# Kernel tuning notes

Measured on AMD Instinct MI355X. Metric: run time of the kernel, lower is better.

## Reference

```python
import jax, jax.numpy as jnp
import numpy as np

N = 50000      # nodes
E = 800000     # edges
IN = 128       # in_feats
HID = 16       # h_feats (per head)
HEADS = 8      # num_heads layer 1
CLS = 40       # num_classes
NEG_SLOPE = 0.2


def setup_inputs() -> dict:
    key = jax.random.key(0)
    ks = jax.random.split(key, 12)
    s = lambda fan: np.float32(1.0 / np.sqrt(fan))
    return {
        "features": jax.random.normal(ks[0], (N, IN), jnp.float32),
        "edge_src": jax.random.randint(ks[1], (E,), 0, N, dtype=jnp.int32),
        "edge_dst": jax.random.randint(ks[2], (E,), 0, N, dtype=jnp.int32),
        # layer 1 params
        "W1": jax.random.normal(ks[3], (IN, HEADS * HID), jnp.float32) * s(IN),
        "al1": jax.random.normal(ks[4], (HEADS, HID), jnp.float32) * s(HID),
        "ar1": jax.random.normal(ks[5], (HEADS, HID), jnp.float32) * s(HID),
        "b1": jnp.zeros((HEADS * HID,), jnp.float32),
        # layer 2 params (1 head)
        "W2": jax.random.normal(ks[6], (HEADS * HID, CLS), jnp.float32) * s(HEADS * HID),
        "al2": jax.random.normal(ks[7], (1, CLS), jnp.float32) * s(CLS),
        "ar2": jax.random.normal(ks[8], (1, CLS), jnp.float32) * s(CLS),
        "b2": jnp.zeros((CLS,), jnp.float32),
    }


def gat_conv(x, W, al, ar, b, src, dst, heads, out_dim):
    # x: [N, F_in] -> feat: [N, H, D]
    feat = (x @ W).reshape(-1, heads, out_dim)
    el = (feat * al).sum(-1)                      # [N, H]
    er = (feat * ar).sum(-1)                      # [N, H]
    e = jax.nn.leaky_relu(el[src] + er[dst], NEG_SLOPE)  # [E, H]
    # segment softmax over destination neighborhoods
    emax = jax.ops.segment_max(e, dst, num_segments=N)   # [N, H]
    emax = jnp.where(jnp.isfinite(emax), emax, jnp.float32(0.0))
    ee = jnp.exp(e - emax[dst])                   # [E, H]
    denom = jax.ops.segment_sum(ee, dst, num_segments=N)
    alpha = ee / (denom[dst] + jnp.float32(1e-9)) # [E, H]
    msg = alpha[:, :, None] * feat[src]           # [E, H, D]
    out = jax.ops.segment_sum(msg, dst, num_segments=N)  # [N, H, D]
    return out + b.reshape(1, heads, out_dim)


def reference(features, edge_src, edge_dst, W1, al1, ar1, b1, W2, al2, ar2, b2):
    h = jax.nn.elu(gat_conv(features, W1, al1, ar1, b1, edge_src, edge_dst, HEADS, HID))
    h = h.reshape(N, HEADS * HID)                 # flatten(1)
    out = gat_conv(h, W2, al2, ar2, b2, edge_src, edge_dst, 1, CLS)
    return out.mean(axis=1)                       # [N, CLS]
```

## Files before the change

### kernel.cpp

```cpp
#include <hip/hip_runtime.h>
#include <hip/hip_bf16.h>

#define N_NODES 50000
#define N_EDGES 800000
#define IN_F    128
#define HID     16
#define HEADS   8
#define F1      128
#define CLS     40
#define CLSP    64
#define NEG     0.2f
#define NEG_INF (-__builtin_inff())
#define SWEEPS      8
#define SWEEP_RANGE 6250
#define STRIDE      96

typedef __bf16 bf16x8 __attribute__((ext_vector_type(8)));
typedef float  f32x4  __attribute__((ext_vector_type(4)));
typedef float  f32x2  __attribute__((ext_vector_type(2)));

__device__ __forceinline__ float leaky(float v) { return v >= 0.0f ? v : NEG * v; }
__device__ __forceinline__ f32x2 unpk(unsigned u) {
    f32x2 r;
    r.x = __uint_as_float(u << 16);
    r.y = __uint_as_float(u & 0xffff0000u);
    return r;
}

__global__ void setup_kernel(const float* __restrict__ W1, const float* __restrict__ W2,
                             __bf16* __restrict__ w1t, __bf16* __restrict__ w2t,
                             int* __restrict__ cursor) {
    int i = blockIdx.x * blockDim.x + threadIdx.x;
    if (i < N_NODES) cursor[i] = 0;
    if (i < 128 * 128) {
        int n = i >> 7, k = i & 127;
        w1t[i] = (__bf16)W1[k * 128 + n];
    }
    if (i < CLSP * 128) {
        int n = i >> 7, k = i & 127;
        w2t[i] = (n < CLS) ? (__bf16)W2[k * CLS + n] : (__bf16)0.0f;
    }
}

__global__ void scatter_kernel(const int* __restrict__ src, const int* __restrict__ dst,
                               int* __restrict__ cursor, int* __restrict__ srcs_sorted) {
    const int BPS = (N_EDGES + 255) / 256;
    int sweep = blockIdx.x / BPS;
    int e = (blockIdx.x - sweep * BPS) * 256 + threadIdx.x;
    if (e >= N_EDGES) return;
    int d = dst[e];
    int lo = sweep * SWEEP_RANGE;
    if (d < lo || d >= lo + SWEEP_RANGE) return;
    int pos = d * STRIDE + atomicAdd(&cursor[d], 1);
    srcs_sorted[pos] = src[e];
}

__global__ __launch_bounds__(256) void gemm1_mfma(const float* __restrict__ A,
                                                  const __bf16* __restrict__ Wt,
                                                  const float* __restrict__ al1,
                                                  const float* __restrict__ ar1,
                                                  __bf16* __restrict__ outb,
                                                  float* __restrict__ el,
                                                  float* __restrict__ er) {
    int wave = threadIdx.x >> 6, lane = threadIdx.x & 63;
    int m0 = blockIdx.x * 64 + wave * 16;
    int c = lane & 15;
    int row = m0 + c;
    int rowc = row < N_NODES ? row : N_NODES - 1;
    int ko = (lane >> 4) * 8;

    f32x4 acc[8];
    #pragma unroll
    for (int t = 0; t < 8; ++t)
        #pragma unroll
        for (int r = 0; r < 4; ++r) acc[t][r] = 0.f;

    for (int ks = 0; ks < 128; ks += 32) {
        const float* ap = A + (size_t)rowc * 128 + ks + ko;
        float4 u = *(const float4*)ap;
        float4 v = *(const float4*)(ap + 4);
        bf16x8 a;
        a[0] = (__bf16)u.x; a[1] = (__bf16)u.y; a[2] = (__bf16)u.z; a[3] = (__bf16)u.w;
        a[4] = (__bf16)v.x; a[5] = (__bf16)v.y; a[6] = (__bf16)v.z; a[7] = (__bf16)v.w;
        #pragma unroll
        for (int t = 0; t < 8; ++t) {
            bf16x8 b = *(const bf16x8*)(Wt + (size_t)(t * 16 + c) * 128 + ks + ko);
            acc[t] = __builtin_amdgcn_mfma_f32_16x16x32_bf16(a, b, acc[t], 0, 0, 0);
        }
    }
    int rbase = m0 + (lane >> 4) * 4;
    #pragma unroll
    for (int t = 0; t < 8; ++t) {
        int gcol = t * 16 + c;
        #pragma unroll
        for (int r = 0; r < 4; ++r) {
            int grow = rbase + r;
            if (grow < N_NODES) outb[(size_t)grow * 128 + gcol] = (__bf16)acc[t][r];
        }
    }
    #pragma unroll
    for (int t = 0; t < 8; ++t) {
        float alv = al1[t * 16 + c];
        float arv = ar1[t * 16 + c];
        float pe[4], pr[4];
        #pragma unroll
        for (int r = 0; r < 4; ++r) { pe[r] = acc[t][r] * alv; pr[r] = acc[t][r] * arv; }
        #pragma unroll
        for (int mask = 1; mask <= 8; mask <<= 1) {
            #pragma unroll
            for (int r = 0; r < 4; ++r) {
                pe[r] += __shfl_xor(pe[r], mask, 64);
                pr[r] += __shfl_xor(pr[r], mask, 64);
            }
        }
        if (c == 0) {
            #pragma unroll
            for (int r = 0; r < 4; ++r) {
                int grow = rbase + r;
                if (grow < N_NODES) {
                    el[grow * 8 + t] = pe[r];
                    er[grow * 8 + t] = pr[r];
                }
            }
        }
    }
}

__global__ __launch_bounds__(256) void gemm2_mfma(const __bf16* __restrict__ A,
                                                  const __bf16* __restrict__ Wt,
                                                  const float* __restrict__ al2,
                                                  const float* __restrict__ ar2,
                                                  __bf16* __restrict__ out,
                                                  float* __restrict__ el,
                                                  float* __restrict__ er) {
    int wave = threadIdx.x >> 6, lane = threadIdx.x & 63;
    int m0 = blockIdx.x * 64 + wave * 16;
    int c = lane & 15;
    int row = m0 + c;
    int rowc = row < N_NODES ? row : N_NODES - 1;
    int ko = (lane >> 4) * 8;

    f32x4 acc[4];
    #pragma unroll
    for (int t = 0; t < 4; ++t)
        #pragma unroll
        for (int r = 0; r < 4; ++r) acc[t][r] = 0.f;

    for (int ks = 0; ks < 128; ks += 32) {
        bf16x8 a = *(const bf16x8*)(A + (size_t)rowc * 128 + ks + ko);
        #pragma unroll
        for (int t = 0; t < 4; ++t) {
            bf16x8 b = *(const bf16x8*)(Wt + (size_t)(t * 16 + c) * 128 + ks + ko);
            acc[t] = __builtin_amdgcn_mfma_f32_16x16x32_bf16(a, b, acc[t], 0, 0, 0);
        }
    }
    int rbase = m0 + (lane >> 4) * 4;
    #pragma unroll
    for (int t = 0; t < 4; ++t) {
        int gcol = t * 16 + c;
        #pragma unroll
        for (int r = 0; r < 4; ++r) {
            int grow = rbase + r;
            if (grow < N_NODES) out[(size_t)grow * CLSP + gcol] = (__bf16)acc[t][r];
        }
    }
    float pe[4] = {0.f, 0.f, 0.f, 0.f}, pr[4] = {0.f, 0.f, 0.f, 0.f};
    #pragma unroll
    for (int t = 0; t < 3; ++t) {
        int idx = t * 16 + c;
        float alv = (idx < CLS) ? al2[idx] : 0.f;
        float arv = (idx < CLS) ? ar2[idx] : 0.f;
        #pragma unroll
        for (int r = 0; r < 4; ++r) { pe[r] += acc[t][r] * alv; pr[r] += acc[t][r] * arv; }
    }
    #pragma unroll
    for (int mask = 1; mask <= 8; mask <<= 1) {
        #pragma unroll
        for (int r = 0; r < 4; ++r) {
            pe[r] += __shfl_xor(pe[r], mask, 64);
            pr[r] += __shfl_xor(pr[r], mask, 64);
        }
    }
    if (c == 0) {
        #pragma unroll
        for (int r = 0; r < 4; ++r) {
            int grow = rbase + r;
            if (grow < N_NODES) { el[grow] = pe[r]; er[grow] = pr[r]; }
        }
    }
}

__global__ __launch_bounds__(256) void gat1_fused(const int* __restrict__ degs,
                                                  const int* __restrict__ srcs,
                                                  const float* __restrict__ el,
                                                  const float* __restrict__ er,
                                                  const __bf16* __restrict__ feat1b,
                                                  const float* __restrict__ b1,
                                                  __bf16* __restrict__ hbufb) {
    __shared__ float a_lds[4][64 * 8];
    __shared__ int   s_lds[4][64];
    int wave = threadIdx.x >> 6;
    int lane = threadIdx.x & 63;
    int d = blockIdx.x * 4 + wave;
    int off = d * STRIDE;
    int deg = degs[d];

    int h = lane & 7, slot = lane >> 3;
    int q = lane >> 4, fg = lane & 15, hd = fg >> 1;
    float er_d = er[d * 8 + h];

    f32x2 accv[4];
    #pragma unroll
    for (int j = 0; j < 4; ++j) { accv[j].x = 0.f; accv[j].y = 0.f; }

    bool fast = (deg <= 64);
    if (fast) {
        int nit = (deg + 7) >> 3;
        float sc[8];
        int sreg[8];
        float m = NEG_INF;
        #pragma unroll
        for (int it = 0; it < 8; ++it) {
            float v = NEG_INF;
            int e = it * 8 + slot;
            if (it < nit && e < deg) {
                sreg[it] = srcs[off + e];
                v = leaky(el[sreg[it] * 8 + h] + er_d);
            }
            sc[it] = v;
            m = fmaxf(m, v);
        }
        float l = 0.f;
        #pragma unroll
        for (int it = 0; it < 8; ++it)
            l += (sc[it] == NEG_INF) ? 0.f : __expf(sc[it] - m);
        #pragma unroll
        for (int mask = 8; mask <= 32; mask <<= 1) {
            float m2 = __shfl_xor(m, mask, 64);
            float l2 = __shfl_xor(l, mask, 64);
            float mn = fmaxf(m, m2);
            float f1 = (m  == NEG_INF) ? 0.f : __expf(m - mn);
            float f2 = (m2 == NEG_INF) ? 0.f : __expf(m2 - mn);
            l = l * f1 + l2 * f2;
            m = mn;
        }
        float inv_l = 1.f / (l + 1e-9f);
        #pragma unroll
        for (int it = 0; it < 8; ++it) {
            int e = it * 8 + slot;
            if (it < nit && e < deg) {
                a_lds[wave][e * 8 + h] = __expf(sc[it] - m) * inv_l;
                if (h == 0) s_lds[wave][e] = sreg[it];
            }
        }
    }
    __syncthreads();

    if (fast) {
        int ng = (deg + 3) >> 2;
        #pragma unroll 4
        for (int g = 0; g < ng; ++g) {
            int k = g * 4 + q;
            float a = 0.f;
            int se = 0;
            if (k < deg) {
                a = a_lds[wave][k * 8 + hd];
                se = s_lds[wave][k];
            }
            uint4 p = *(const uint4*)(feat1b + (size_t)se * F1 + fg * 8);
            f32x2 av; av.x = a; av.y = a;
            accv[0] += av * unpk(p.x);
            accv[1] += av * unpk(p.y);
            accv[2] += av * unpk(p.z);
            accv[3] += av * unpk(p.w);
        }
    } else {
        float m = NEG_INF, l = 0.f;
        for (int base = 0; base < deg; base += 8) {
            int e = base + slot;
            float v = NEG_INF;
            if (e < deg) {
                int s = srcs[off + e];
                v = leaky(el[s * 8 + h] + er_d);
            }
            float mn = fmaxf(m, v);
            float f1 = (m == NEG_INF) ? 0.f : __expf(m - mn);
            float f2 = (v == NEG_INF) ? 0.f : __expf(v - mn);
            l = l * f1 + f2;
            m = mn;
        }
        #pragma unroll
        for (int mask = 8; mask <= 32; mask <<= 1) {
            float m2 = __shfl_xor(m, mask, 64);
            float l2 = __shfl_xor(l, mask, 64);
            float mn = fmaxf(m, m2);
            float f1 = (m  == NEG_INF) ? 0.f : __expf(m - mn);
            float f2 = (m2 == NEG_INF) ? 0.f : __expf(m2 - mn);
            l = l * f1 + l2 * f2;
            m = mn;
        }
        float inv_l = 1.f / (l + 1e-9f);

        for (int base = 0; base < deg; base += 8) {
            int e = base + slot;
            float alpha = 0.f;
            int s = 0;
            if (e < deg) {
                s = srcs[off + e];
                float v = leaky(el[s * 8 + h] + er_d);
                alpha = __expf(v - m) * inv_l;
            }
            #pragma unroll
            for (int sub = 0; sub < 2; ++sub) {
                int k = sub * 4 + q;
                float a  = __shfl(alpha, k * 8 + hd, 64);
                int   se = __shfl(s,     k * 8,      64);
                uint4 p = *(const uint4*)(feat1b + (size_t)se * F1 + fg * 8);
                f32x2 av; av.x = a; av.y = a;
                accv[0] += av * unpk(p.x);
                accv[1] += av * unpk(p.y);
                accv[2] += av * unpk(p.z);
                accv[3] += av * unpk(p.w);
            }
        }
    }

    float acc[8];
    #pragma unroll
    for (int j = 0; j < 4; ++j) { acc[2 * j] = accv[j].x; acc[2 * j + 1] = accv[j].y; }
    #pragma unroll
    for (int i = 0; i < 8; ++i) {
        acc[i] += __shfl_xor(acc[i], 16, 64);
        acc[i] += __shfl_xor(acc[i], 32, 64);
    }
    if (q == 0) {
        bf16x8 o;
        #pragma unroll
        for (int i = 0; i < 8; ++i) {
            float v = acc[i] + b1[fg * 8 + i];
            v = v > 0.f ? v : expm1f(v);
            o[i] = (__bf16)v;
        }
        *(bf16x8*)(hbufb + (size_t)d * F1 + fg * 8) = o;
    }
}

__global__ __launch_bounds__(256) void gat2_fused(const int* __restrict__ degs,
                                                  const int* __restrict__ srcs,
                                                  const float* __restrict__ el,
                                                  const float* __restrict__ er,
                                                  const __bf16* __restrict__ feat2p,
                                                  const float* __restrict__ b2,
                                                  float* __restrict__ out) {
    __shared__ float a_lds[4][64];
    __shared__ int   s_lds[4][64];
    int wave = threadIdx.x >> 6;
    int lane = threadIdx.x & 63;
    int d = blockIdx.x * 4 + wave;
    int off = d * STRIDE;
    int deg = degs[d];

    float er_d = er[d];
    bool fast = (deg <= 64);
    if (fast) {
        float sc = NEG_INF;
        int s0 = 0;
        if (lane < deg) {
            s0 = srcs[off + lane];
            sc = leaky(el[s0] + er_d);
        }
        float m = sc, l = (sc == NEG_INF) ? 0.f : 1.f;
        #pragma unroll
        for (int mask = 1; mask <= 32; mask <<= 1) {
            float m2 = __shfl_xor(m, mask, 64);
            float l2 = __shfl_xor(l, mask, 64);
            float mn = fmaxf(m, m2);
            float f1 = (m  == NEG_INF) ? 0.f : __expf(m - mn);
            float f2 = (m2 == NEG_INF) ? 0.f : __expf(m2 - mn);
            l = l * f1 + l2 * f2;
            m = mn;
        }
        float inv_l = 1.f / (l + 1e-9f);
        if (lane < deg) {
            a_lds[wave][lane] = __expf(sc - m) * inv_l;
            s_lds[wave][lane] = s0;
        }
    }
    __syncthreads();

    if (fast) {
        int q2  = lane >> 3;
        int cg8 = lane & 7;
        f32x2 accv[4];
        #pragma unroll
        for (int j = 0; j < 4; ++j) { accv[j].x = 0.f; accv[j].y = 0.f; }

        int ng = (deg + 7) >> 3;
        #pragma unroll 4
        for (int g = 0; g < ng; ++g) {
            int k = g * 8 + q2;
            float a = 0.f;
            int se = 0;
            if (k < deg) {
                a = a_lds[wave][k];
                se = s_lds[wave][k];
            }
            uint4 p = *(const uint4*)(feat2p + (size_t)se * CLSP + cg8 * 8);
            f32x2 av; av.x = a; av.y = a;
            accv[0] += av * unpk(p.x);
            accv[1] += av * unpk(p.y);
            accv[2] += av * unpk(p.z);
            accv[3] += av * unpk(p.w);
        }
        float acc[8];
        #pragma unroll
        for (int j = 0; j < 4; ++j) { acc[2 * j] = accv[j].x; acc[2 * j + 1] = accv[j].y; }
        #pragma unroll
        for (int i = 0; i < 8; ++i) {
            acc[i] += __shfl_xor(acc[i], 8, 64);
            acc[i] += __shfl_xor(acc[i], 16, 64);
            acc[i] += __shfl_xor(acc[i], 32, 64);
        }
        if (q2 == 0 && cg8 < 5) {
            float4 o0, o1;
            o0.x = acc[0] + b2[cg8 * 8 + 0];
            o0.y = acc[1] + b2[cg8 * 8 + 1];
            o0.z = acc[2] + b2[cg8 * 8 + 2];
            o0.w = acc[3] + b2[cg8 * 8 + 3];
            o1.x = acc[4] + b2[cg8 * 8 + 4];
            o1.y = acc[5] + b2[cg8 * 8 + 5];
            o1.z = acc[6] + b2[cg8 * 8 + 6];
            o1.w = acc[7] + b2[cg8 * 8 + 7];
            *(float4*)(out + (size_t)d * CLS + cg8 * 8)     = o0;
            *(float4*)(out + (size_t)d * CLS + cg8 * 8 + 4) = o1;
        }
    } else {
        int q  = lane >> 4;
        int cg = lane & 15;
        f32x2 accv[2];
        accv[0].x = 0.f; accv[0].y = 0.f; accv[1].x = 0.f; accv[1].y = 0.f;

        float m = NEG_INF, l = 0.f;
        for (int base = 0; base < deg; base += 64) {
            int e = base + lane;
            float sc = NEG_INF;
            if (e < deg) {
                int s = srcs[off + e];
                sc = leaky(el[s] + er_d);
            }
            float mn = fmaxf(m, sc);
            float f1 = (m  == NEG_INF) ? 0.f : __expf(m - mn);
            float f2 = (sc == NEG_INF) ? 0.f : __expf(sc - mn);
            l = l * f1 + f2;
            m = mn;
        }
        #pragma unroll
        for (int mask = 1; mask <= 32; mask <<= 1) {
            float m2 = __shfl_xor(m, mask, 64);
            float l2 = __shfl_xor(l, mask, 64);
            float mn = fmaxf(m, m2);
            float f1 = (m  == NEG_INF) ? 0.f : __expf(m - mn);
            float f2 = (m2 == NEG_INF) ? 0.f : __expf(m2 - mn);
            l = l * f1 + l2 * f2;
            m = mn;
        }
        float inv_l = 1.f / (l + 1e-9f);

        for (int base = 0; base < deg; base += 64) {
            int e = base + lane;
            float alpha = 0.f;
            int s = 0;
            if (e < deg) {
                s = srcs[off + e];
                float sc = leaky(el[s] + er_d);
                alpha = __expf(sc - m) * inv_l;
            }
            int kmax = min(64, deg - base);
            int nsub = (kmax + 3) >> 2;
            for (int sub = 0; sub < nsub; ++sub) {
                int k = sub * 4 + q;
                float a  = __shfl(alpha, k, 64);
                int   se = __shfl(s,     k, 64);
                uint2 p = *(const uint2*)(feat2p + (size_t)se * CLSP + cg * 4);
                f32x2 av; av.x = a; av.y = a;
                accv[0] += av * unpk(p.x);
                accv[1] += av * unpk(p.y);
            }
        }
        float acc[4];
        acc[0] = accv[0].x; acc[1] = accv[0].y; acc[2] = accv[1].x; acc[3] = accv[1].y;
        #pragma unroll
        for (int i = 0; i < 4; ++i) {
            acc[i] += __shfl_xor(acc[i], 16, 64);
            acc[i] += __shfl_xor(acc[i], 32, 64);
        }
        if (lane < 10) {
            float4 o;
            o.x = acc[0] + b2[cg * 4 + 0];
            o.y = acc[1] + b2[cg * 4 + 1];
            o.z = acc[2] + b2[cg * 4 + 2];
            o.w = acc[3] + b2[cg * 4 + 3];
            *(float4*)(out + (size_t)d * CLS + cg * 4) = o;
        }
    }
}

extern "C" void kernel_launch(void* const* d_in, const int* in_sizes, int n_in,
                              void* d_out, int out_size, void* d_ws, size_t ws_size,
                              hipStream_t stream) {
    const float* features = (const float*)d_in[0];
    const int*   esrc     = (const int*)d_in[1];
    const int*   edst     = (const int*)d_in[2];
    const float* W1       = (const float*)d_in[3];
    const float* al1      = (const float*)d_in[4];
    const float* ar1      = (const float*)d_in[5];
    const float* b1       = (const float*)d_in[6];
    const float* W2       = (const float*)d_in[7];
    const float* al2      = (const float*)d_in[8];
    const float* ar2      = (const float*)d_in[9];
    const float* b2       = (const float*)d_in[10];
    float* out = (float*)d_out;

    float* ws = (float*)d_ws;
    float*  el1    = ws;
    float*  er1    = ws + 400000;
    float*  el2    = ws + 800000;
    float*  er2    = ws + 850000;
    int*    cursor = (int*)(ws + 900000);
    int*    srcs   = (int*)(ws + 950000);
    __bf16* feat1b = (__bf16*)(ws + 5750000);
    __bf16* hbufb  = (__bf16*)(ws + 8950000);
    __bf16* feat2p = (__bf16*)(ws + 12150000);
    __bf16* w1t    = (__bf16*)(ws + 13750000);
    __bf16* w2t    = (__bf16*)(ws + 13760000);

    const int B = 256;
    const int BPS = (N_EDGES + 255) / 256;

    setup_kernel<<<(N_NODES + B - 1) / B, B, 0, stream>>>(W1, W2, w1t, w2t, cursor);
    scatter_kernel<<<SWEEPS * BPS, B, 0, stream>>>(esrc, edst, cursor, srcs);

    gemm1_mfma<<<(N_NODES + 63) / 64, 256, 0, stream>>>(features, w1t, al1, ar1,
                                                        feat1b, el1, er1);
    gat1_fused<<<N_NODES / 4, B, 0, stream>>>(cursor, srcs, el1, er1, feat1b, b1, hbufb);

    gemm2_mfma<<<(N_NODES + 63) / 64, 256, 0, stream>>>(hbufb, w2t, al2, ar2,
                                                        feat2p, el2, er2);
    gat2_fused<<<N_NODES / 4, B, 0, stream>>>(cursor, srcs, el2, er2, feat2p, b2, out);
}
```

Baseline: 271.7 us.

## Fuse edge scatter with gemm1 and fold gemm2 into gat1 epilogue

The edge-bucketing scatter and the first-layer GEMM now run as one launch, with blocks partitioned by index, so the two independent jobs can overlap. The second-layer projection (W2 matmul plus el2/er2 attention logits) moves into the gat1 aggregation epilogue. W2 is staged in LDS per block and reduced with wave shuffles, which drops the hidden-activation buffer round trip and two kernel launches. In exchange the MFMA GEMM becomes scalar FMAs with extra shuffle reductions and a per-block W2 copy into LDS, and gat1 uses more LDS.

```diff
diff --git a/kernel.cpp b/kernel.cpp
--- a/kernel.cpp
+++ b/kernel.cpp
@@ -14,6 +14,8 @@
 #define SWEEPS      8
 #define SWEEP_RANGE 6250
 #define STRIDE      96
+#define BPS         3125
+#define G1B         782
 
 typedef __bf16 bf16x8 __attribute__((ext_vector_type(8)));
 typedef float  f32x4  __attribute__((ext_vector_type(4)));
@@ -42,26 +44,29 @@
     }
 }
 
-__global__ void scatter_kernel(const int* __restrict__ src, const int* __restrict__ dst,
-                               int* __restrict__ cursor, int* __restrict__ srcs_sorted) {
-    const int BPS = (N_EDGES + 255) / 256;
-    int sweep = blockIdx.x / BPS;
-    int e = (blockIdx.x - sweep * BPS) * 256 + threadIdx.x;
-    if (e >= N_EDGES) return;
-    int d = dst[e];
-    int lo = sweep * SWEEP_RANGE;
-    if (d < lo || d >= lo + SWEEP_RANGE) return;
-    int pos = d * STRIDE + atomicAdd(&cursor[d], 1);
-    srcs_sorted[pos] = src[e];
-}
-
-__global__ __launch_bounds__(256) void gemm1_mfma(const float* __restrict__ A,
-                                                  const __bf16* __restrict__ Wt,
-                                                  const float* __restrict__ al1,
-                                                  const float* __restrict__ ar1,
-                                                  __bf16* __restrict__ outb,
-                                                  float* __restrict__ el,
-                                                  float* __restrict__ er) {
+__global__ __launch_bounds__(256) void scatter_gemm1(const int* __restrict__ esrc,
+                                                     const int* __restrict__ edst,
+                                                     int* __restrict__ cursor,
+                                                     int* __restrict__ srcs_sorted,
+                                                     const float* __restrict__ A,
+                                                     const __bf16* __restrict__ Wt,
+                                                     const float* __restrict__ al1,
+                                                     const float* __restrict__ ar1,
+                                                     __bf16* __restrict__ outb,
+                                                     float* __restrict__ el,
+                                                     float* __restrict__ er) {
+    if (blockIdx.x >= G1B) {
+        int b = blockIdx.x - G1B;
+        int sweep = b / BPS;
+        int e = (b - sweep * BPS) * 256 + threadIdx.x;
+        if (e >= N_EDGES) return;
+        int d = edst[e];
+        int lo = sweep * SWEEP_RANGE;
+        if (d < lo || d >= lo + SWEEP_RANGE) return;
+        int pos = d * STRIDE + atomicAdd(&cursor[d], 1);
+        srcs_sorted[pos] = esrc[e];
+        return;
+    }
     int wave = threadIdx.x >> 6, lane = threadIdx.x & 63;
     int m0 = blockIdx.x * 64 + wave * 16;
     int c = lane & 15;
@@ -126,84 +131,29 @@
     }
 }
 
-__global__ __launch_bounds__(256) void gemm2_mfma(const __bf16* __restrict__ A,
-                                                  const __bf16* __restrict__ Wt,
-                                                  const float* __restrict__ al2,
-                                                  const float* __restrict__ ar2,
-                                                  __bf16* __restrict__ out,
-                                                  float* __restrict__ el,
-                                                  float* __restrict__ er) {
-    int wave = threadIdx.x >> 6, lane = threadIdx.x & 63;
-    int m0 = blockIdx.x * 64 + wave * 16;
-    int c = lane & 15;
-    int row = m0 + c;
-    int rowc = row < N_NODES ? row : N_NODES - 1;
-    int ko = (lane >> 4) * 8;
-
-    f32x4 acc[4];
-    #pragma unroll
-    for (int t = 0; t < 4; ++t)
-        #pragma unroll
-        for (int r = 0; r < 4; ++r) acc[t][r] = 0.f;
-
-    for (int ks = 0; ks < 128; ks += 32) {
-        bf16x8 a = *(const bf16x8*)(A + (size_t)rowc * 128 + ks + ko);
-        #pragma unroll
-        for (int t = 0; t < 4; ++t) {
-            bf16x8 b = *(const bf16x8*)(Wt + (size_t)(t * 16 + c) * 128 + ks + ko);
-            acc[t] = __builtin_amdgcn_mfma_f32_16x16x32_bf16(a, b, acc[t], 0, 0, 0);
-        }
-    }
-    int rbase = m0 + (lane >> 4) * 4;
-    #pragma unroll
-    for (int t = 0; t < 4; ++t) {
-        int gcol = t * 16 + c;
-        #pragma unroll
-        for (int r = 0; r < 4; ++r) {
-            int grow = rbase + r;
-            if (grow < N_NODES) out[(size_t)grow * CLSP + gcol] = (__bf16)acc[t][r];
-        }
-    }
-    float pe[4] = {0.f, 0.f, 0.f, 0.f}, pr[4] = {0.f, 0.f, 0.f, 0.f};
-    #pragma unroll
-    for (int t = 0; t < 3; ++t) {
-        int idx = t * 16 + c;
-        float alv = (idx < CLS) ? al2[idx] : 0.f;
-        float arv = (idx < CLS) ? ar2[idx] : 0.f;
-        #pragma unroll
-        for (int r = 0; r < 4; ++r) { pe[r] += acc[t][r] * alv; pr[r] += acc[t][r] * arv; }
-    }
-    #pragma unroll
-    for (int mask = 1; mask <= 8; mask <<= 1) {
-        #pragma unroll
-        for (int r = 0; r < 4; ++r) {
-            pe[r] += __shfl_xor(pe[r], mask, 64);
-            pr[r] += __shfl_xor(pr[r], mask, 64);
-        }
-    }
-    if (c == 0) {
-        #pragma unroll
-        for (int r = 0; r < 4; ++r) {
-            int grow = rbase + r;
-            if (grow < N_NODES) { el[grow] = pe[r]; er[grow] = pr[r]; }
-        }
-    }
-}
-
 __global__ __launch_bounds__(256) void gat1_fused(const int* __restrict__ degs,
                                                   const int* __restrict__ srcs,
                                                   const float* __restrict__ el,
                                                   const float* __restrict__ er,
                                                   const __bf16* __restrict__ feat1b,
                                                   const float* __restrict__ b1,
-                                                  __bf16* __restrict__ hbufb) {
-    __shared__ float a_lds[4][64 * 8];
-    __shared__ int   s_lds[4][64];
+                                                  const __bf16* __restrict__ w2t,
+                                                  const float* __restrict__ al2,
+                                                  const float* __restrict__ ar2,
+                                                  __bf16* __restrict__ feat2p,
+                                                  float* __restrict__ el2,
+                                                  float* __restrict__ er2) {
+    __shared__ float  a_lds[4][64 * 8];
+    __shared__ int    s_lds[4][64];
+    __shared__ __bf16 w2_lds[CLS * 128];
     int wave = threadIdx.x >> 6;
     int lane = threadIdx.x & 63;
     int d = blockIdx.x * 4 + wave;
     int off = d * STRIDE;
     int deg = degs[d];
+
+    for (int i = threadIdx.x; i < CLS * 128 / 8; i += 256)
+        ((uint4*)w2_lds)[i] = ((const uint4*)w2t)[i];
 
     int h = lane & 7, slot = lane >> 3;
     int q = lane >> 4, fg = lane & 15, hd = fg >> 1;
@@ -333,16 +283,42 @@
         acc[i] += __shfl_xor(acc[i], 16, 64);
         acc[i] += __shfl_xor(acc[i], 32, 64);
     }
-    if (q == 0) {
-        bf16x8 o;
-        #pragma unroll
-        for (int i = 0; i < 8; ++i) {
-            float v = acc[i] + b1[fg * 8 + i];
-            v = v > 0.f ? v : expm1f(v);
-            o[i] = (__bf16)v;
-        }
-        *(bf16x8*)(hbufb + (size_t)d * F1 + fg * 8) = o;
-    }
+    float hrow[8];
+    #pragma unroll
+    for (int i = 0; i < 8; ++i) {
+        float v = acc[i] + b1[fg * 8 + i];
+        hrow[i] = v > 0.f ? v : expm1f(v);
+    }
+    float f2o[10];
+    #pragma unroll
+    for (int ci = 0; ci < 10; ++ci) {
+        int cc = q * 10 + ci;
+        bf16x8 w = *(const bf16x8*)&w2_lds[cc * 128 + fg * 8];
+        float s = 0.f;
+        #pragma unroll
+        for (int j = 0; j < 8; ++j) s += hrow[j] * (float)w[j];
+        f2o[ci] = s;
+    }
+    #pragma unroll
+    for (int mask = 1; mask <= 8; mask <<= 1)
+        #pragma unroll
+        for (int ci = 0; ci < 10; ++ci)
+            f2o[ci] += __shfl_xor(f2o[ci], mask, 64);
+    if (fg == 0) {
+        #pragma unroll
+        for (int ci = 0; ci < 10; ++ci)
+            feat2p[(size_t)d * CLSP + q * 10 + ci] = (__bf16)f2o[ci];
+    }
+    float pe = 0.f, pr = 0.f;
+    #pragma unroll
+    for (int ci = 0; ci < 10; ++ci) {
+        int cc = q * 10 + ci;
+        pe += f2o[ci] * al2[cc];
+        pr += f2o[ci] * ar2[cc];
+    }
+    pe += __shfl_xor(pe, 16, 64); pe += __shfl_xor(pe, 32, 64);
+    pr += __shfl_xor(pr, 16, 64); pr += __shfl_xor(pr, 32, 64);
+    if (lane == 0) { el2[d] = pe; er2[d] = pr; }
 }
 
 __global__ __launch_bounds__(256) void gat2_fused(const int* __restrict__ degs,
@@ -529,22 +505,17 @@
     int*    cursor = (int*)(ws + 900000);
     int*    srcs   = (int*)(ws + 950000);
     __bf16* feat1b = (__bf16*)(ws + 5750000);
-    __bf16* hbufb  = (__bf16*)(ws + 8950000);
-    __bf16* feat2p = (__bf16*)(ws + 12150000);
-    __bf16* w1t    = (__bf16*)(ws + 13750000);
-    __bf16* w2t    = (__bf16*)(ws + 13760000);
+    __bf16* feat2p = (__bf16*)(ws + 8950000);
+    __bf16* w1t    = (__bf16*)(ws + 10550000);
+    __bf16* w2t    = (__bf16*)(ws + 10560000);
 
     const int B = 256;
-    const int BPS = (N_EDGES + 255) / 256;
 
     setup_kernel<<<(N_NODES + B - 1) / B, B, 0, stream>>>(W1, W2, w1t, w2t, cursor);
-    scatter_kernel<<<SWEEPS * BPS, B, 0, stream>>>(esrc, edst, cursor, srcs);
-
-    gemm1_mfma<<<(N_NODES + 63) / 64, 256, 0, stream>>>(features, w1t, al1, ar1,
+    scatter_gemm1<<<G1B + SWEEPS * BPS, B, 0, stream>>>(esrc, edst, cursor, srcs,
+                                                        features, w1t, al1, ar1,
                                                         feat1b, el1, er1);
-    gat1_fused<<<N_NODES / 4, B, 0, stream>>>(cursor, srcs, el1, er1, feat1b, b1, hbufb);
-
-    gemm2_mfma<<<(N_NODES + 63) / 64, 256, 0, stream>>>(hbufb, w2t, al2, ar2,
-                                                        feat2p, el2, er2);
+    gat1_fused<<<N_NODES / 4, B, 0, stream>>>(cursor, srcs, el1, er1, feat1b, b1,
+                                              w2t, al2, ar2, feat2p, el2, er2);
     gat2_fused<<<N_NODES / 4, B, 0, stream>>>(cursor, srcs, el2, er2, feat2p, b2, out);
 }
```

New measurement: 276.7 us. No clear change (+1.9%).
